# Performance work log

Measured on AMD Instinct MI355X. Metric: run time of the kernel, lower is better.

Reference implementation:

```python
import jax, jax.numpy as jnp
import numpy as np

D_MODEL = 1024
B, S = 4, 4096


def setup_inputs() -> dict:
    key = jax.random.key(0)
    k1, k2, k3, k4, k5 = jax.random.split(key, 5)
    lim = 1.0 / np.sqrt(D_MODEL)  # nn.Linear default init range
    x = jax.random.normal(k1, (B, S, D_MODEL), dtype=jnp.float32)
    mask = jnp.ones((B, S), dtype=jnp.float32)
    W_up = jax.random.uniform(k2, (D_MODEL, D_MODEL), jnp.float32, -lim, lim)
    b_up = jax.random.uniform(k3, (D_MODEL,), jnp.float32, -lim, lim)
    W_f = jax.random.uniform(k4, (D_MODEL, D_MODEL), jnp.float32, -lim, lim)
    b_f = jax.random.uniform(k5, (D_MODEL,), jnp.float32, -lim, lim)
    decay_param = jnp.zeros((1,), dtype=jnp.float32)
    return {"x": x, "mask": mask, "W_up": W_up, "b_up": b_up,
            "W_f": W_f, "b_f": b_f, "decay_param": decay_param}


def _decay_scan(u, decay):
    # h_t = decay * h_{t-1} + u_t  along axis=1, via associative scan.
    # Element: (a, b) representing h -> a*h + b; compose: (a1*a2, b1*a2 + b2).
    a = jnp.broadcast_to(decay, u.shape)

    def combine(c1, c2):
        a1, b1 = c1
        a2, b2 = c2
        return a1 * a2, b1 * a2 + b2

    _, h = jax.lax.associative_scan(combine, (a, u), axis=1)
    return h


def reference(x, mask, W_up, b_up, W_f, b_f, decay_param):
    decay = jax.nn.sigmoid(decay_param)[0]
    # u_i = mask_i * linear_update(x_i)
    u = (jnp.einsum('bsd,ed->bse', x, W_up) + b_up) * mask[..., None]
    # h_t = sum_{i<=t} decay^(t-i) * u_i  (exponential-decay recurrence)
    h = _decay_scan(u, decay)
    return jnp.einsum('bsd,ed->bse', h, W_f) + b_f
```

## Files before the change

kernel.cpp:

```cpp
#include <hip/hip_runtime.h>
#include <hip/hip_bf16.h>
#include <cstdint>
#include <cstddef>

#define DMODEL 1024
#define BATCH  4
#define SEQ    4096
#define BSROWS (BATCH*SEQ)
#define CHUNK  16
#define NCHUNK (SEQ/CHUNK)
#define NCH_T  (BATCH*NCHUNK)

typedef __attribute__((ext_vector_type(8))) short bf16x8;
typedef __attribute__((ext_vector_type(4))) float f32x4;


__device__ __forceinline__ unsigned short f2bf(float f) {
  union { float f; uint32_t u; } v; v.f = f;
  uint32_t u = v.u;
  u += 0x7FFFu + ((u >> 16) & 1u);
  return (unsigned short)(u >> 16);
}

__device__ __forceinline__ float sigmoid_dev(const float* dp) {
  return 1.0f / (1.0f + expf(-dp[0]));
}

typedef __attribute__((address_space(1))) void void_g;
typedef __attribute__((address_space(3))) void void_l;

__device__ __forceinline__ void gl2lds16(const void* g, void* l) {
  __builtin_amdgcn_global_load_lds((void_g*)g, (void_l*)l, 16, 0, 0);
}

__device__ __forceinline__ void kloop64(
    const unsigned short* __restrict__ A, const unsigned short* __restrict__ B,
    int m0, int n0, f32x4 acc[2][2],
    unsigned short* As, unsigned short* Bs, int tid) {
  int lane = tid & 63, w = tid >> 6, wm = w & 1, wn = w >> 1;
  int quad = lane >> 4, l16 = lane & 15;
  int r = tid >> 3, cch = tid & 7;
  int g = cch ^ (r & 7);

  auto stage = [&](int t, int slot) {
    int k0 = t * 64;
    unsigned short* dA = As + slot * 4096;
    unsigned short* dB = Bs + slot * 4096;
    gl2lds16(A + (size_t)(m0 + r) * DMODEL + k0 + g * 8,      dA + r * 64 + cch * 8);
    gl2lds16(A + (size_t)(m0 + 32 + r) * DMODEL + k0 + g * 8, dA + (32 + r) * 64 + cch * 8);
    gl2lds16(B + (size_t)(n0 + r) * DMODEL + k0 + g * 8,      dB + r * 64 + cch * 8);
    gl2lds16(B + (size_t)(n0 + 32 + r) * DMODEL + k0 + g * 8, dB + (32 + r) * 64 + cch * 8);
  };
  auto compute = [&](int slot) {
    const bf16x8* Av = (const bf16x8*)(As + slot * 4096);
    const bf16x8* Bv = (const bf16x8*)(Bs + slot * 4096);
    #pragma unroll
    for (int kk = 0; kk < 2; ++kk) {
      bf16x8 af[2], bfr[2];
      #pragma unroll
      for (int i = 0; i < 2; ++i) {
        int rowA = wm * 32 + i * 16 + l16;
        af[i]  = Av[rowA * 8 + ((kk * 4 + quad) ^ (l16 & 7))];
        int rowB = wn * 32 + i * 16 + l16;
        bfr[i] = Bv[rowB * 8 + ((kk * 4 + quad) ^ (l16 & 7))];
      }
      __builtin_amdgcn_s_setprio(1);
      #pragma unroll
      for (int i = 0; i < 2; ++i)
        #pragma unroll
        for (int j = 0; j < 2; ++j)
          acc[i][j] = __builtin_amdgcn_mfma_f32_16x16x32_bf16(af[i], bfr[j], acc[i][j], 0, 0, 0);
      __builtin_amdgcn_s_setprio(0);
    }
  };

  stage(0, 0); stage(1, 1);
  asm volatile("s_waitcnt vmcnt(4)" ::: "memory");
  __builtin_amdgcn_s_barrier();
  asm volatile("" ::: "memory");
  int cur = 0;
  for (int t = 0; t < 14; ++t) {
    int ns = cur + 2; if (ns >= 3) ns -= 3;
    stage(t + 2, ns);
    compute(cur);
    asm volatile("s_waitcnt vmcnt(4)" ::: "memory");
    __builtin_amdgcn_s_barrier();
    asm volatile("" ::: "memory");
    cur = (cur == 2) ? 0 : cur + 1;
  }
  compute(cur);
  asm volatile("s_waitcnt vmcnt(0)" ::: "memory");
  __builtin_amdgcn_s_barrier();
  asm volatile("" ::: "memory");
  cur = (cur == 2) ? 0 : cur + 1;
  compute(cur);
}

__global__ __launch_bounds__(256) void prep_scan(
    const float* __restrict__ x, const float* __restrict__ mask,
    const float* __restrict__ dp,
    unsigned short* __restrict__ hv, float* __restrict__ carry,
    float* __restrict__ lbeta, float* __restrict__ cbeta) {
  int blk = blockIdx.x;
  int tid = threadIdx.x;
  float decay = sigmoid_dev(dp);
  int b = blk >> 8, c = blk & 255;
  int base = b * SEQ + c * CHUNK;
  const float4* xp = (const float4*)(x + (size_t)base * DMODEL);
  const float4* mp4 = (const float4*)(mask + base);
  float mreg[16];
  #pragma unroll
  for (int q = 0; q < 4; ++q) {
    float4 t = mp4[q];
    mreg[q * 4 + 0] = t.x; mreg[q * 4 + 1] = t.y;
    mreg[q * 4 + 2] = t.z; mreg[q * 4 + 3] = t.w;
  }

  {
    float hb = 0.f;
    #pragma unroll
    for (int i = 0; i < 16; ++i) {
      float nv = decay * hb + mreg[i];
      hb = (tid >= i) ? nv : hb;
    }
    if (tid < 16) {
      lbeta[base + tid] = hb;
      if (tid == 15) cbeta[blk] = hb;
    }
  }

  float4 x0 = xp[tid];
  float4 x1 = xp[256 + tid];
  float4 h = make_float4(0.f, 0.f, 0.f, 0.f);
  #pragma unroll
  for (int s = 0; s < CHUNK; ++s) {
    float4 cur = x0;
    x0 = x1;
    if (s + 2 < CHUNK) x1 = xp[(size_t)(s + 2) * 256 + tid];
    float m = mreg[s];
    h.x = decay * h.x + m * cur.x;
    h.y = decay * h.y + m * cur.y;
    h.z = decay * h.z + m * cur.z;
    h.w = decay * h.w + m * cur.w;
    ushort4 o;
    o.x = f2bf(h.x); o.y = f2bf(h.y); o.z = f2bf(h.z); o.w = f2bf(h.w);
    ((ushort4*)hv)[(size_t)(base + s) * 256 + tid] = o;
  }
  ((float4*)carry)[(size_t)blk * 256 + tid] = h;
}

__global__ __launch_bounds__(256) void prep_misc(
    const float* __restrict__ W_up, const float* __restrict__ b_up,
    const float* __restrict__ W_f,
    unsigned short* __restrict__ Wf_bf, unsigned short* __restrict__ WupT,
    float* __restrict__ bb) {
  __shared__ float tile[32][33];
  int blk = blockIdx.x;
  int tid = threadIdx.x;
  if (blk < 256) {
    int w = tid >> 6, lane = tid & 63;
    int e = blk * 4 + w;
    const float4* row4 = (const float4*)(W_f + (size_t)e * DMODEL);
    const float4* bup4 = (const float4*)b_up;
    ushort4* out4 = (ushort4*)(Wf_bf + (size_t)e * DMODEL);
    float s = 0.f;
    #pragma unroll
    for (int q = 0; q < 4; ++q) {
      float4 v  = row4[q * 64 + lane];
      float4 bu = bup4[q * 64 + lane];
      ushort4 o;
      o.x = f2bf(v.x); o.y = f2bf(v.y); o.z = f2bf(v.z); o.w = f2bf(v.w);
      out4[q * 64 + lane] = o;
      s += v.x * bu.x + v.y * bu.y + v.z * bu.z + v.w * bu.w;
    }
    #pragma unroll
    for (int off = 32; off; off >>= 1) s += __shfl_down(s, off);
    if (lane == 0) bb[e] = s;
  } else {
    int id = blk - 256;
    int bx = id & 31, by = id >> 5;
    int tx = tid & 31, ty = tid >> 5;
    int xx = bx * 32 + tx;
    int y0 = by * 32;
    for (int j = ty; j < 32; j += 8)
      tile[j][tx] = W_up[(size_t)(y0 + j) * DMODEL + xx];
    __syncthreads();
    int dd = tid >> 3;
    int c4 = (tid & 7) * 4;
    ushort4 o;
    o.x = f2bf(tile[c4 + 0][dd]);
    o.y = f2bf(tile[c4 + 1][dd]);
    o.z = f2bf(tile[c4 + 2][dd]);
    o.w = f2bf(tile[c4 + 3][dd]);
    *(ushort4*)(WupT + (size_t)(bx * 32 + dd) * DMODEL + y0 + c4) = o;
  }
}

__global__ __launch_bounds__(256) void mid2_kernel(
    const unsigned short* __restrict__ Wf_bf,
    const unsigned short* __restrict__ WupT,
    unsigned short* __restrict__ Wc,
    const float* __restrict__ carry, const float* __restrict__ cbeta,
    const float* __restrict__ dp,
    unsigned short* __restrict__ Pbf, float* __restrict__ pbeta) {
  __shared__ unsigned short As[3 * 64 * 64];
  __shared__ unsigned short Bs[3 * 64 * 64];
  int tid = threadIdx.x;
  if (blockIdx.x < 256) {
    int mt = blockIdx.x >> 4, nt = blockIdx.x & 15;
    f32x4 acc[2][2] = {};
    kloop64(Wf_bf, WupT, mt * 64, nt * 64, acc, As, Bs, tid);
    int lane = tid & 63, w = tid >> 6, wm = w & 1, wn = w >> 1;
    int quad = lane >> 4, l16 = lane & 15;
    #pragma unroll
    for (int j = 0; j < 2; ++j) {
      int col = nt * 64 + wn * 32 + j * 16 + l16;
      #pragma unroll
      for (int i = 0; i < 2; ++i) {
        int rowb = mt * 64 + wm * 32 + i * 16 + quad * 4;
        #pragma unroll
        for (int rr = 0; rr < 4; ++rr)
          Wc[(size_t)(rowb + rr) * DMODEL + col] = f2bf(acc[i][j][rr]);
      }
    }
  } else {
    float decay = sigmoid_dev(dp);
    float dL = powf(decay, (float)CHUNK);
    int gid = (blockIdx.x - 256) * 256 + tid;
    int b = gid >> 10, dd = gid & 1023;
    float P = 0.f;
    for (int c0 = 0; c0 < NCHUNK; c0 += 8) {
      float v[8];
      #pragma unroll
      for (int j = 0; j < 8; ++j)
        v[j] = carry[(size_t)(b * NCHUNK + c0 + j) * DMODEL + dd];
      #pragma unroll
      for (int j = 0; j < 8; ++j) {
        Pbf[(size_t)(b * NCHUNK + c0 + j) * DMODEL + dd] = f2bf(P);
        P = dL * P + v[j];
      }
    }
    if (dd == 0) {
      float Pb = 0.f;
      for (int c0 = 0; c0 < NCHUNK; c0 += 16) {
        float v[16];
        #pragma unroll
        for (int j = 0; j < 16; ++j) v[j] = cbeta[b * NCHUNK + c0 + j];
        #pragma unroll
        for (int j = 0; j < 16; ++j) {
          pbeta[b * NCHUNK + c0 + j] = Pb;
          Pb = dL * Pb + v[j];
        }
      }
    }
  }
}

__global__ __launch_bounds__(512) void gemm_main(
    const unsigned short* __restrict__ A,
    const unsigned short* __restrict__ Bm,
    const unsigned short* __restrict__ Pbf,
    const float* __restrict__ pbeta,
    const float* __restrict__ lbeta,
    const float* __restrict__ bb,
    const float* __restrict__ bias_f,
    const float* __restrict__ dp,
    float* __restrict__ out) {
  __shared__ unsigned short As[2 * 256 * 64];
  __shared__ unsigned short Bs[2 * 256 * 64];
  __shared__ unsigned short Ps[2 * 16 * 64];
  __shared__ float dpow[CHUNK];
  const int TSLOT = 256 * 64;
  const int PSLOT = 16 * 64;
  int tid = threadIdx.x;
  if (tid < CHUNK) {
    float decay = sigmoid_dev(dp);
    dpow[tid] = powf(decay, (float)(tid + 1));
  }

  int lane = tid & 63, wid = tid >> 6;
  int wm = wid >> 2, wn = wid & 3;
  int quad = lane >> 4, l16 = lane & 15;
  int r = tid >> 3, cch = tid & 7;
  int g = cch ^ (r & 7);

  int bid = blockIdx.x;
  int xcd = bid & 7, jb = bid >> 3;
  int m0 = (xcd * 8 + (jb >> 2)) * 256;
  int n0 = (jb & 3) * 256;
  int chunk0 = m0 >> 4;

  f32x4 acc[8][4] = {};
  f32x4 Pacc[4] = {};

  auto stageT = [&](int t, int p) {
    int k0 = t * 64;
    unsigned short* dA = As + p * TSLOT;
    unsigned short* dB = Bs + p * TSLOT;
    #pragma unroll
    for (int q = 0; q < 4; ++q)
      gl2lds16(A + (size_t)(m0 + q * 64 + r) * DMODEL + k0 + g * 8,
               dA + (q * 64 + r) * 64 + cch * 8);
    #pragma unroll
    for (int q = 0; q < 4; ++q)
      gl2lds16(Bm + (size_t)(n0 + q * 64 + r) * DMODEL + k0 + g * 8,
               dB + (q * 64 + r) * 64 + cch * 8);
    if (wid < 2) {
      int rp = wid * 8 + (lane >> 3), cp = lane & 7;
      int gp = cp ^ (rp & 7);
      gl2lds16(Pbf + (size_t)(chunk0 + rp) * DMODEL + k0 + gp * 8,
               Ps + p * PSLOT + (wid * 64 + lane) * 8);
    }
  };
  auto compute = [&](int p) {
    const bf16x8* Av = (const bf16x8*)(As + p * TSLOT);
    const bf16x8* Bv = (const bf16x8*)(Bs + p * TSLOT);
    const bf16x8* Pv = (const bf16x8*)(Ps + p * PSLOT);
    #pragma unroll
    for (int kk = 0; kk < 2; ++kk) {
      bf16x8 bfr[4];
      #pragma unroll
      for (int j = 0; j < 4; ++j) {
        int rowB = wn * 64 + j * 16 + l16;
        bfr[j] = Bv[rowB * 8 + ((kk * 4 + quad) ^ (l16 & 7))];
      }
      bf16x8 pf = Pv[l16 * 8 + ((kk * 4 + quad) ^ (l16 & 7))];
      __builtin_amdgcn_s_setprio(1);
      #pragma unroll
      for (int j = 0; j < 4; ++j)
        Pacc[j] = __builtin_amdgcn_mfma_f32_16x16x32_bf16(pf, bfr[j], Pacc[j], 0, 0, 0);
      __builtin_amdgcn_s_setprio(0);
      #pragma unroll
      for (int i = 0; i < 8; ++i) {
        int rowA = wm * 128 + i * 16 + l16;
        bf16x8 af = Av[rowA * 8 + ((kk * 4 + quad) ^ (l16 & 7))];
        __builtin_amdgcn_s_setprio(1);
        #pragma unroll
        for (int j = 0; j < 4; ++j)
          acc[i][j] = __builtin_amdgcn_mfma_f32_16x16x32_bf16(af, bfr[j], acc[i][j], 0, 0, 0);
        __builtin_amdgcn_s_setprio(0);
      }
    }
  };

  stageT(0, 0);
  __syncthreads();

  for (int t = 0; t < 15; ++t) {
    int p = t & 1;
    stageT(t + 1, p ^ 1);
    compute(p);
    asm volatile("s_waitcnt vmcnt(0)" ::: "memory");
    __builtin_amdgcn_s_barrier();
    asm volatile("" ::: "memory");
  }
  compute(1);

  float* Plds = (float*)As;
  if (wm == 0) {
    #pragma unroll
    for (int j = 0; j < 4; ++j)
      #pragma unroll
      for (int rr = 0; rr < 4; ++rr)
        Plds[(quad * 4 + rr) * 256 + wn * 64 + j * 16 + l16] = Pacc[j][rr];
  }
  __syncthreads();

  float bbv[4], bfv[4];
  #pragma unroll
  for (int j = 0; j < 4; ++j) {
    int col = n0 + wn * 64 + j * 16 + l16;
    bbv[j] = bb[col];
    bfv[j] = bias_f[col];
  }
  #pragma unroll
  for (int i = 0; i < 8; ++i) {
    int chl = wm * 8 + i;
    float pb = pbeta[chunk0 + chl];
    #pragma unroll
    for (int rr = 0; rr < 4; ++rr) {
      int row = m0 + wm * 128 + i * 16 + quad * 4 + rr;
      float lb  = lbeta[row];
      float dpw = dpow[row & (CHUNK - 1)];
      float* outRow = out + (size_t)row * DMODEL;
      #pragma unroll
      for (int j = 0; j < 4; ++j) {
        int col = n0 + wn * 64 + j * 16 + l16;
        float po = Plds[chl * 256 + wn * 64 + j * 16 + l16] + pb * bbv[j];
        outRow[col] = acc[i][j][rr] + dpw * po + lb * bbv[j] + bfv[j];
      }
    }
  }
}


extern "C" void kernel_launch(void* const* d_in, const int* in_sizes, int n_in,
                              void* d_out, int out_size, void* d_ws, size_t ws_size,
                              hipStream_t stream) {
  const float* x    = (const float*)d_in[0];
  const float* mask = (const float*)d_in[1];
  const float* W_up = (const float*)d_in[2];
  const float* b_up = (const float*)d_in[3];
  const float* W_f  = (const float*)d_in[4];
  const float* b_f  = (const float*)d_in[5];
  const float* dp   = (const float*)d_in[6];
  float* out = (float*)d_out;

  char* ws = (char*)d_ws;
  unsigned short* hv    = (unsigned short*)(ws);
  unsigned short* Wc    = (unsigned short*)(ws + 33554432);
  unsigned short* Wf_bf = (unsigned short*)(ws + 35651584);
  unsigned short* WupT  = (unsigned short*)(ws + 37748736);
  float* carry  = (float*)(ws + 39845888);
  unsigned short* Pbf = (unsigned short*)(ws + 44040192);
  float* lbeta  = (float*)(ws + 46137344);
  float* cbeta  = (float*)(ws + 46202880);
  float* pbeta  = (float*)(ws + 46206976);
  float* bb     = (float*)(ws + 46211072);

  prep_scan<<<1024, 256, 0, stream>>>(x, mask, dp, hv, carry, lbeta, cbeta);
  prep_misc<<<1280, 256, 0, stream>>>(W_up, b_up, W_f, Wf_bf, WupT, bb);
  mid2_kernel<<<272, 256, 0, stream>>>(Wf_bf, WupT, Wc, carry, cbeta, dp,
                                       Pbf, pbeta);
  gemm_main<<<256, 512, 0, stream>>>(hv, Wc, Pbf, pbeta, lbeta, bb, b_f, dp, out);
}
```

Measured before the change: 195.9 us.

## Fuse all four stages into one cooperative persistent kernel with grid syncs

Merges the four separate launches (scan prep, weight prep, weight-combine GEMM plus carry scan, main GEMM) into a single cooperative kernel of 256 blocks of 512 threads, with grid.sync between phases. The goal is to remove launch gaps and tail effects between the small kernels. It also replaces the serial per-batch pbeta scan with a warp-level parallel scan and deepens the x prefetch in the chunk scan from 2 to 4 rows. The cost is fewer concurrent blocks in the prep phases (256 instead of 1024 or 1280), two grid-wide barriers, and the constraint that all blocks must be co-resident.

```diff
diff --git a/kernel.cpp b/kernel.cpp
--- a/kernel.cpp
+++ b/kernel.cpp
@@ -1,7 +1,10 @@
 #include <hip/hip_runtime.h>
+#include <hip/hip_cooperative_groups.h>
 #include <hip/hip_bf16.h>
 #include <cstdint>
 #include <cstddef>
+
+namespace cg = cooperative_groups;
 
 #define DMODEL 1024
 #define BATCH  4
@@ -96,15 +99,12 @@
   compute(cur);
 }
 
-__global__ __launch_bounds__(256) void prep_scan(
+__device__ __forceinline__ void scan_chunk(
+    int ch, int ltid, float decay,
     const float* __restrict__ x, const float* __restrict__ mask,
-    const float* __restrict__ dp,
     unsigned short* __restrict__ hv, float* __restrict__ carry,
     float* __restrict__ lbeta, float* __restrict__ cbeta) {
-  int blk = blockIdx.x;
-  int tid = threadIdx.x;
-  float decay = sigmoid_dev(dp);
-  int b = blk >> 8, c = blk & 255;
+  int b = ch >> 8, c = ch & 255;
   int base = b * SEQ + c * CHUNK;
   const float4* xp = (const float4*)(x + (size_t)base * DMODEL);
   const float4* mp4 = (const float4*)(mask + base);
@@ -115,28 +115,24 @@
     mreg[q * 4 + 0] = t.x; mreg[q * 4 + 1] = t.y;
     mreg[q * 4 + 2] = t.z; mreg[q * 4 + 3] = t.w;
   }
-
   {
     float hb = 0.f;
     #pragma unroll
     for (int i = 0; i < 16; ++i) {
       float nv = decay * hb + mreg[i];
-      hb = (tid >= i) ? nv : hb;
-    }
-    if (tid < 16) {
-      lbeta[base + tid] = hb;
-      if (tid == 15) cbeta[blk] = hb;
-    }
-  }
-
-  float4 x0 = xp[tid];
-  float4 x1 = xp[256 + tid];
+      hb = (ltid >= i) ? nv : hb;
+    }
+    if (ltid < 16) {
+      lbeta[base + ltid] = hb;
+      if (ltid == 15) cbeta[ch] = hb;
+    }
+  }
+  float4 x0 = xp[ltid], x1 = xp[256 + ltid], x2 = xp[512 + ltid], x3 = xp[768 + ltid];
   float4 h = make_float4(0.f, 0.f, 0.f, 0.f);
   #pragma unroll
   for (int s = 0; s < CHUNK; ++s) {
-    float4 cur = x0;
-    x0 = x1;
-    if (s + 2 < CHUNK) x1 = xp[(size_t)(s + 2) * 256 + tid];
+    float4 cur = x0; x0 = x1; x1 = x2; x2 = x3;
+    if (s + 4 < CHUNK) x3 = xp[(size_t)(s + 4) * 256 + ltid];
     float m = mreg[s];
     h.x = decay * h.x + m * cur.x;
     h.y = decay * h.y + m * cur.y;
@@ -144,127 +140,21 @@
     h.w = decay * h.w + m * cur.w;
     ushort4 o;
     o.x = f2bf(h.x); o.y = f2bf(h.y); o.z = f2bf(h.z); o.w = f2bf(h.w);
-    ((ushort4*)hv)[(size_t)(base + s) * 256 + tid] = o;
-  }
-  ((float4*)carry)[(size_t)blk * 256 + tid] = h;
-}
-
-__global__ __launch_bounds__(256) void prep_misc(
+    ((ushort4*)hv)[(size_t)(base + s) * 256 + ltid] = o;
+  }
+  ((float4*)carry)[(size_t)ch * 256 + ltid] = h;
+}
+
+__global__ __launch_bounds__(512) void mega(
+    const float* __restrict__ x, const float* __restrict__ mask,
     const float* __restrict__ W_up, const float* __restrict__ b_up,
-    const float* __restrict__ W_f,
+    const float* __restrict__ W_f, const float* __restrict__ bias_f,
+    const float* __restrict__ dp,
+    unsigned short* __restrict__ hv, float* __restrict__ carry,
     unsigned short* __restrict__ Wf_bf, unsigned short* __restrict__ WupT,
-    float* __restrict__ bb) {
-  __shared__ float tile[32][33];
-  int blk = blockIdx.x;
-  int tid = threadIdx.x;
-  if (blk < 256) {
-    int w = tid >> 6, lane = tid & 63;
-    int e = blk * 4 + w;
-    const float4* row4 = (const float4*)(W_f + (size_t)e * DMODEL);
-    const float4* bup4 = (const float4*)b_up;
-    ushort4* out4 = (ushort4*)(Wf_bf + (size_t)e * DMODEL);
-    float s = 0.f;
-    #pragma unroll
-    for (int q = 0; q < 4; ++q) {
-      float4 v  = row4[q * 64 + lane];
-      float4 bu = bup4[q * 64 + lane];
-      ushort4 o;
-      o.x = f2bf(v.x); o.y = f2bf(v.y); o.z = f2bf(v.z); o.w = f2bf(v.w);
-      out4[q * 64 + lane] = o;
-      s += v.x * bu.x + v.y * bu.y + v.z * bu.z + v.w * bu.w;
-    }
-    #pragma unroll
-    for (int off = 32; off; off >>= 1) s += __shfl_down(s, off);
-    if (lane == 0) bb[e] = s;
-  } else {
-    int id = blk - 256;
-    int bx = id & 31, by = id >> 5;
-    int tx = tid & 31, ty = tid >> 5;
-    int xx = bx * 32 + tx;
-    int y0 = by * 32;
-    for (int j = ty; j < 32; j += 8)
-      tile[j][tx] = W_up[(size_t)(y0 + j) * DMODEL + xx];
-    __syncthreads();
-    int dd = tid >> 3;
-    int c4 = (tid & 7) * 4;
-    ushort4 o;
-    o.x = f2bf(tile[c4 + 0][dd]);
-    o.y = f2bf(tile[c4 + 1][dd]);
-    o.z = f2bf(tile[c4 + 2][dd]);
-    o.w = f2bf(tile[c4 + 3][dd]);
-    *(ushort4*)(WupT + (size_t)(bx * 32 + dd) * DMODEL + y0 + c4) = o;
-  }
-}
-
-__global__ __launch_bounds__(256) void mid2_kernel(
-    const unsigned short* __restrict__ Wf_bf,
-    const unsigned short* __restrict__ WupT,
-    unsigned short* __restrict__ Wc,
-    const float* __restrict__ carry, const float* __restrict__ cbeta,
-    const float* __restrict__ dp,
-    unsigned short* __restrict__ Pbf, float* __restrict__ pbeta) {
-  __shared__ unsigned short As[3 * 64 * 64];
-  __shared__ unsigned short Bs[3 * 64 * 64];
-  int tid = threadIdx.x;
-  if (blockIdx.x < 256) {
-    int mt = blockIdx.x >> 4, nt = blockIdx.x & 15;
-    f32x4 acc[2][2] = {};
-    kloop64(Wf_bf, WupT, mt * 64, nt * 64, acc, As, Bs, tid);
-    int lane = tid & 63, w = tid >> 6, wm = w & 1, wn = w >> 1;
-    int quad = lane >> 4, l16 = lane & 15;
-    #pragma unroll
-    for (int j = 0; j < 2; ++j) {
-      int col = nt * 64 + wn * 32 + j * 16 + l16;
-      #pragma unroll
-      for (int i = 0; i < 2; ++i) {
-        int rowb = mt * 64 + wm * 32 + i * 16 + quad * 4;
-        #pragma unroll
-        for (int rr = 0; rr < 4; ++rr)
-          Wc[(size_t)(rowb + rr) * DMODEL + col] = f2bf(acc[i][j][rr]);
-      }
-    }
-  } else {
-    float decay = sigmoid_dev(dp);
-    float dL = powf(decay, (float)CHUNK);
-    int gid = (blockIdx.x - 256) * 256 + tid;
-    int b = gid >> 10, dd = gid & 1023;
-    float P = 0.f;
-    for (int c0 = 0; c0 < NCHUNK; c0 += 8) {
-      float v[8];
-      #pragma unroll
-      for (int j = 0; j < 8; ++j)
-        v[j] = carry[(size_t)(b * NCHUNK + c0 + j) * DMODEL + dd];
-      #pragma unroll
-      for (int j = 0; j < 8; ++j) {
-        Pbf[(size_t)(b * NCHUNK + c0 + j) * DMODEL + dd] = f2bf(P);
-        P = dL * P + v[j];
-      }
-    }
-    if (dd == 0) {
-      float Pb = 0.f;
-      for (int c0 = 0; c0 < NCHUNK; c0 += 16) {
-        float v[16];
-        #pragma unroll
-        for (int j = 0; j < 16; ++j) v[j] = cbeta[b * NCHUNK + c0 + j];
-        #pragma unroll
-        for (int j = 0; j < 16; ++j) {
-          pbeta[b * NCHUNK + c0 + j] = Pb;
-          Pb = dL * Pb + v[j];
-        }
-      }
-    }
-  }
-}
-
-__global__ __launch_bounds__(512) void gemm_main(
-    const unsigned short* __restrict__ A,
-    const unsigned short* __restrict__ Bm,
-    const unsigned short* __restrict__ Pbf,
-    const float* __restrict__ pbeta,
-    const float* __restrict__ lbeta,
-    const float* __restrict__ bb,
-    const float* __restrict__ bias_f,
-    const float* __restrict__ dp,
+    unsigned short* __restrict__ Wc, unsigned short* __restrict__ Pbf,
+    float* __restrict__ lbeta, float* __restrict__ cbeta,
+    float* __restrict__ pbeta, float* __restrict__ bb,
     float* __restrict__ out) {
   __shared__ unsigned short As[2 * 256 * 64];
   __shared__ unsigned short Bs[2 * 256 * 64];
@@ -273,121 +163,261 @@
   const int TSLOT = 256 * 64;
   const int PSLOT = 16 * 64;
   int tid = threadIdx.x;
-  if (tid < CHUNK) {
-    float decay = sigmoid_dev(dp);
-    dpow[tid] = powf(decay, (float)(tid + 1));
-  }
-
-  int lane = tid & 63, wid = tid >> 6;
-  int wm = wid >> 2, wn = wid & 3;
-  int quad = lane >> 4, l16 = lane & 15;
-  int r = tid >> 3, cch = tid & 7;
-  int g = cch ^ (r & 7);
-
-  int bid = blockIdx.x;
-  int xcd = bid & 7, jb = bid >> 3;
-  int m0 = (xcd * 8 + (jb >> 2)) * 256;
-  int n0 = (jb & 3) * 256;
-  int chunk0 = m0 >> 4;
-
-  f32x4 acc[8][4] = {};
-  f32x4 Pacc[4] = {};
-
-  auto stageT = [&](int t, int p) {
-    int k0 = t * 64;
-    unsigned short* dA = As + p * TSLOT;
-    unsigned short* dB = Bs + p * TSLOT;
+  int blk = blockIdx.x;
+  float decay = sigmoid_dev(dp);
+  cg::grid_group grid = cg::this_grid();
+
+  {
+    int g = tid >> 8;
+    int ltid = tid & 255;
+    scan_chunk(blk * 4 + g * 2 + 0, ltid, decay, x, mask, hv, carry, lbeta, cbeta);
+    scan_chunk(blk * 4 + g * 2 + 1, ltid, decay, x, mask, hv, carry, lbeta, cbeta);
+
+    if (tid < 256) {
+      int w = tid >> 6, lane = tid & 63;
+      int e = blk * 4 + w;
+      const float4* row4 = (const float4*)(W_f + (size_t)e * DMODEL);
+      const float4* bup4 = (const float4*)b_up;
+      ushort4* out4 = (ushort4*)(Wf_bf + (size_t)e * DMODEL);
+      float s = 0.f;
+      #pragma unroll
+      for (int q = 0; q < 4; ++q) {
+        float4 v  = row4[q * 64 + lane];
+        float4 bu = bup4[q * 64 + lane];
+        ushort4 o;
+        o.x = f2bf(v.x); o.y = f2bf(v.y); o.z = f2bf(v.z); o.w = f2bf(v.w);
+        out4[q * 64 + lane] = o;
+        s += v.x * bu.x + v.y * bu.y + v.z * bu.z + v.w * bu.w;
+      }
+      #pragma unroll
+      for (int off = 32; off; off >>= 1) s += __shfl_down(s, off);
+      if (lane == 0) bb[e] = s;
+    } else {
+      int wv = (tid >> 6) - 4, lane = tid & 63;
+      int id = blk * 4 + wv;
+      int bx = id & 31, by = id >> 5;
+      int x0c = bx * 32, y0 = by * 32;
+      float* tw = (float*)As + wv * (32 * 33);
+      #pragma unroll
+      for (int p = 0; p < 4; ++p) {
+        int idx = p * 64 + lane;
+        int rr = idx >> 3, q = idx & 7;
+        float4 t = *(const float4*)(W_up + (size_t)(y0 + rr) * DMODEL + x0c + q * 4);
+        tw[rr * 33 + q * 4 + 0] = t.x;
+        tw[rr * 33 + q * 4 + 1] = t.y;
+        tw[rr * 33 + q * 4 + 2] = t.z;
+        tw[rr * 33 + q * 4 + 3] = t.w;
+      }
+      asm volatile("s_waitcnt lgkmcnt(0)" ::: "memory");
+      __builtin_amdgcn_sched_barrier(0);
+      #pragma unroll
+      for (int p = 0; p < 4; ++p) {
+        int idx = p * 64 + lane;
+        int d = idx >> 3, q = idx & 7;
+        ushort4 o;
+        o.x = f2bf(tw[(q * 4 + 0) * 33 + d]);
+        o.y = f2bf(tw[(q * 4 + 1) * 33 + d]);
+        o.z = f2bf(tw[(q * 4 + 2) * 33 + d]);
+        o.w = f2bf(tw[(q * 4 + 3) * 33 + d]);
+        *(ushort4*)(WupT + (size_t)(x0c + d) * DMODEL + y0 + q * 4) = o;
+      }
+    }
+  }
+  __syncthreads();
+  __threadfence();
+  grid.sync();
+  __threadfence();
+
+  {
+    unsigned short* As2 = As;
+    unsigned short* Bs2 = As + 3 * 4096;
+    if (tid < 256) {
+      int mt = blk >> 4, nt = blk & 15;
+      f32x4 acc[2][2] = {};
+      kloop64(Wf_bf, WupT, mt * 64, nt * 64, acc, As2, Bs2, tid);
+      int lane = tid & 63, w = tid >> 6, wm = w & 1, wn = w >> 1;
+      int quad = lane >> 4, l16 = lane & 15;
+      #pragma unroll
+      for (int j = 0; j < 2; ++j) {
+        int col = nt * 64 + wn * 32 + j * 16 + l16;
+        #pragma unroll
+        for (int i = 0; i < 2; ++i) {
+          int rowb = mt * 64 + wm * 32 + i * 16 + quad * 4;
+          #pragma unroll
+          for (int rr = 0; rr < 4; ++rr)
+            Wc[(size_t)(rowb + rr) * DMODEL + col] = f2bf(acc[i][j][rr]);
+        }
+      }
+    } else {
+      float dL = powf(decay, (float)CHUNK);
+      if (blk < 16) {
+        int gid = blk * 256 + (tid - 256);
+        int b = gid >> 10, dd = gid & 1023;
+        float P = 0.f;
+        for (int c0 = 0; c0 < NCHUNK; c0 += 8) {
+          float v[8];
+          #pragma unroll
+          for (int j = 0; j < 8; ++j)
+            v[j] = carry[(size_t)(b * NCHUNK + c0 + j) * DMODEL + dd];
+          #pragma unroll
+          for (int j = 0; j < 8; ++j) {
+            Pbf[(size_t)(b * NCHUNK + c0 + j) * DMODEL + dd] = f2bf(P);
+            P = dL * P + v[j];
+          }
+          if (c0 & 8) __builtin_amdgcn_s_barrier();
+        }
+      } else if (blk == 16) {
+        int wv = (tid >> 6) - 4, lane = tid & 63;
+        float F = dL * dL; F = F * F;
+        float c0v = cbeta[wv * NCHUNK + lane * 4 + 0];
+        float c1v = cbeta[wv * NCHUNK + lane * 4 + 1];
+        float c2v = cbeta[wv * NCHUNK + lane * 4 + 2];
+        float c3v = cbeta[wv * NCHUNK + lane * 4 + 3];
+        float p1 = c0v;
+        float p2 = dL * p1 + c1v;
+        float p3 = dL * p2 + c2v;
+        float T  = dL * p3 + c3v;
+        float s = T, f = F;
+        #pragma unroll
+        for (int off = 1; off < 64; off <<= 1) {
+          float u = __shfl_up(s, off);
+          if (lane >= off) s += f * u;
+          f = f * f;
+        }
+        float E = __shfl_up(s, 1);
+        if (lane == 0) E = 0.f;
+        float q0 = E;
+        float q1 = dL * q0 + c0v;
+        float q2 = dL * q1 + c1v;
+        float q3 = dL * q2 + c2v;
+        pbeta[wv * NCHUNK + lane * 4 + 0] = q0;
+        pbeta[wv * NCHUNK + lane * 4 + 1] = q1;
+        pbeta[wv * NCHUNK + lane * 4 + 2] = q2;
+        pbeta[wv * NCHUNK + lane * 4 + 3] = q3;
+        for (int i = 0; i < 16; ++i) __builtin_amdgcn_s_barrier();
+      } else {
+        for (int i = 0; i < 16; ++i) __builtin_amdgcn_s_barrier();
+      }
+    }
+  }
+  __syncthreads();
+  __threadfence();
+  grid.sync();
+  __threadfence();
+
+  {
+    if (tid < CHUNK) dpow[tid] = powf(decay, (float)(tid + 1));
+
+    int lane = tid & 63, wid = tid >> 6;
+    int wm = wid >> 2, wn = wid & 3;
+    int quad = lane >> 4, l16 = lane & 15;
+    int r = tid >> 3, cch = tid & 7;
+    int g = cch ^ (r & 7);
+
+    int xcd = blk & 7, jb = blk >> 3;
+    int m0 = (xcd * 8 + (jb >> 2)) * 256;
+    int n0 = (jb & 3) * 256;
+    int chunk0 = m0 >> 4;
+
+    f32x4 acc[8][4] = {};
+    f32x4 Pacc[4] = {};
+
+    auto stageT = [&](int t, int p) {
+      int k0 = t * 64;
+      unsigned short* dA = As + p * TSLOT;
+      unsigned short* dB = Bs + p * TSLOT;
+      #pragma unroll
+      for (int q = 0; q < 4; ++q)
+        gl2lds16(hv + (size_t)(m0 + q * 64 + r) * DMODEL + k0 + g * 8,
+                 dA + (q * 64 + r) * 64 + cch * 8);
+      #pragma unroll
+      for (int q = 0; q < 4; ++q)
+        gl2lds16(Wc + (size_t)(n0 + q * 64 + r) * DMODEL + k0 + g * 8,
+                 dB + (q * 64 + r) * 64 + cch * 8);
+      if (wid < 2) {
+        int rp = wid * 8 + (lane >> 3), cp = lane & 7;
+        int gp = cp ^ (rp & 7);
+        gl2lds16(Pbf + (size_t)(chunk0 + rp) * DMODEL + k0 + gp * 8,
+                 Ps + p * PSLOT + (wid * 64 + lane) * 8);
+      }
+    };
+    auto compute = [&](int p) {
+      const bf16x8* Av = (const bf16x8*)(As + p * TSLOT);
+      const bf16x8* Bv = (const bf16x8*)(Bs + p * TSLOT);
+      const bf16x8* Pv = (const bf16x8*)(Ps + p * PSLOT);
+      #pragma unroll
+      for (int kk = 0; kk < 2; ++kk) {
+        bf16x8 bfr[4];
+        #pragma unroll
+        for (int j = 0; j < 4; ++j) {
+          int rowB = wn * 64 + j * 16 + l16;
+          bfr[j] = Bv[rowB * 8 + ((kk * 4 + quad) ^ (l16 & 7))];
+        }
+        bf16x8 pf = Pv[l16 * 8 + ((kk * 4 + quad) ^ (l16 & 7))];
+        __builtin_amdgcn_s_setprio(1);
+        #pragma unroll
+        for (int j = 0; j < 4; ++j)
+          Pacc[j] = __builtin_amdgcn_mfma_f32_16x16x32_bf16(pf, bfr[j], Pacc[j], 0, 0, 0);
+        __builtin_amdgcn_s_setprio(0);
+        #pragma unroll
+        for (int i = 0; i < 8; ++i) {
+          int rowA = wm * 128 + i * 16 + l16;
+          bf16x8 af = Av[rowA * 8 + ((kk * 4 + quad) ^ (l16 & 7))];
+          __builtin_amdgcn_s_setprio(1);
+          #pragma unroll
+          for (int j = 0; j < 4; ++j)
+            acc[i][j] = __builtin_amdgcn_mfma_f32_16x16x32_bf16(af, bfr[j], acc[i][j], 0, 0, 0);
+          __builtin_amdgcn_s_setprio(0);
+        }
+      }
+    };
+
+    stageT(0, 0);
+    __syncthreads();
+
+    for (int t = 0; t < 15; ++t) {
+      int p = t & 1;
+      stageT(t + 1, p ^ 1);
+      compute(p);
+      asm volatile("s_waitcnt vmcnt(0)" ::: "memory");
+      __builtin_amdgcn_s_barrier();
+      asm volatile("" ::: "memory");
+    }
+    compute(1);
+
+    float* Plds = (float*)As;
+    if (wm == 0) {
+      #pragma unroll
+      for (int j = 0; j < 4; ++j)
+        #pragma unroll
+        for (int rr = 0; rr < 4; ++rr)
+          Plds[(quad * 4 + rr) * 256 + wn * 64 + j * 16 + l16] = Pacc[j][rr];
+    }
+    __syncthreads();
+
+    float bbv[4], bfv[4];
     #pragma unroll
-    for (int q = 0; q < 4; ++q)
-      gl2lds16(A + (size_t)(m0 + q * 64 + r) * DMODEL + k0 + g * 8,
-               dA + (q * 64 + r) * 64 + cch * 8);
+    for (int j = 0; j < 4; ++j) {
+      int col = n0 + wn * 64 + j * 16 + l16;
+      bbv[j] = bb[col];
+      bfv[j] = bias_f[col];
+    }
     #pragma unroll
-    for (int q = 0; q < 4; ++q)
-      gl2lds16(Bm + (size_t)(n0 + q * 64 + r) * DMODEL + k0 + g * 8,
-               dB + (q * 64 + r) * 64 + cch * 8);
-    if (wid < 2) {
-      int rp = wid * 8 + (lane >> 3), cp = lane & 7;
-      int gp = cp ^ (rp & 7);
-      gl2lds16(Pbf + (size_t)(chunk0 + rp) * DMODEL + k0 + gp * 8,
-               Ps + p * PSLOT + (wid * 64 + lane) * 8);
-    }
-  };
-  auto compute = [&](int p) {
-    const bf16x8* Av = (const bf16x8*)(As + p * TSLOT);
-    const bf16x8* Bv = (const bf16x8*)(Bs + p * TSLOT);
-    const bf16x8* Pv = (const bf16x8*)(Ps + p * PSLOT);
-    #pragma unroll
-    for (int kk = 0; kk < 2; ++kk) {
-      bf16x8 bfr[4];
-      #pragma unroll
-      for (int j = 0; j < 4; ++j) {
-        int rowB = wn * 64 + j * 16 + l16;
-        bfr[j] = Bv[rowB * 8 + ((kk * 4 + quad) ^ (l16 & 7))];
-      }
-      bf16x8 pf = Pv[l16 * 8 + ((kk * 4 + quad) ^ (l16 & 7))];
-      __builtin_amdgcn_s_setprio(1);
-      #pragma unroll
-      for (int j = 0; j < 4; ++j)
-        Pacc[j] = __builtin_amdgcn_mfma_f32_16x16x32_bf16(pf, bfr[j], Pacc[j], 0, 0, 0);
-      __builtin_amdgcn_s_setprio(0);
-      #pragma unroll
-      for (int i = 0; i < 8; ++i) {
-        int rowA = wm * 128 + i * 16 + l16;
-        bf16x8 af = Av[rowA * 8 + ((kk * 4 + quad) ^ (l16 & 7))];
-        __builtin_amdgcn_s_setprio(1);
-        #pragma unroll
-        for (int j = 0; j < 4; ++j)
-          acc[i][j] = __builtin_amdgcn_mfma_f32_16x16x32_bf16(af, bfr[j], acc[i][j], 0, 0, 0);
-        __builtin_amdgcn_s_setprio(0);
-      }
-    }
-  };
-
-  stageT(0, 0);
-  __syncthreads();
-
-  for (int t = 0; t < 15; ++t) {
-    int p = t & 1;
-    stageT(t + 1, p ^ 1);
-    compute(p);
-    asm volatile("s_waitcnt vmcnt(0)" ::: "memory");
-    __builtin_amdgcn_s_barrier();
-    asm volatile("" ::: "memory");
-  }
-  compute(1);
-
-  float* Plds = (float*)As;
-  if (wm == 0) {
-    #pragma unroll
-    for (int j = 0; j < 4; ++j)
-      #pragma unroll
-      for (int rr = 0; rr < 4; ++rr)
-        Plds[(quad * 4 + rr) * 256 + wn * 64 + j * 16 + l16] = Pacc[j][rr];
-  }
-  __syncthreads();
-
-  float bbv[4], bfv[4];
-  #pragma unroll
-  for (int j = 0; j < 4; ++j) {
-    int col = n0 + wn * 64 + j * 16 + l16;
-    bbv[j] = bb[col];
-    bfv[j] = bias_f[col];
-  }
-  #pragma unroll
-  for (int i = 0; i < 8; ++i) {
-    int chl = wm * 8 + i;
-    float pb = pbeta[chunk0 + chl];
-    #pragma unroll
-    for (int rr = 0; rr < 4; ++rr) {
-      int row = m0 + wm * 128 + i * 16 + quad * 4 + rr;
-      float lb  = lbeta[row];
-      float dpw = dpow[row & (CHUNK - 1)];
-      float* outRow = out + (size_t)row * DMODEL;
-      #pragma unroll
-      for (int j = 0; j < 4; ++j) {
-        int col = n0 + wn * 64 + j * 16 + l16;
-        float po = Plds[chl * 256 + wn * 64 + j * 16 + l16] + pb * bbv[j];
-        outRow[col] = acc[i][j][rr] + dpw * po + lb * bbv[j] + bfv[j];
+    for (int i = 0; i < 8; ++i) {
+      int chl = wm * 8 + i;
+      float pb = pbeta[chunk0 + chl];
+      #pragma unroll
+      for (int rr = 0; rr < 4; ++rr) {
+        int row = m0 + wm * 128 + i * 16 + quad * 4 + rr;
+        float lb  = lbeta[row];
+        float dpw = dpow[row & (CHUNK - 1)];
+        float* outRow = out + (size_t)row * DMODEL;
+        #pragma unroll
+        for (int j = 0; j < 4; ++j) {
+          int col = n0 + wn * 64 + j * 16 + l16;
+          float po = Plds[chl * 256 + wn * 64 + j * 16 + l16] + pb * bbv[j];
+          outRow[col] = acc[i][j][rr] + dpw * po + lb * bbv[j] + bfv[j];
+        }
       }
     }
   }
@@ -418,9 +448,13 @@
   float* pbeta  = (float*)(ws + 46206976);
   float* bb     = (float*)(ws + 46211072);
 
-  prep_scan<<<1024, 256, 0, stream>>>(x, mask, dp, hv, carry, lbeta, cbeta);
-  prep_misc<<<1280, 256, 0, stream>>>(W_up, b_up, W_f, Wf_bf, WupT, bb);
-  mid2_kernel<<<272, 256, 0, stream>>>(Wf_bf, WupT, Wc, carry, cbeta, dp,
-                                       Pbf, pbeta);
-  gemm_main<<<256, 512, 0, stream>>>(hv, Wc, Pbf, pbeta, lbeta, bb, b_f, dp, out);
-}
+  void* kargs[] = {
+    (void*)&x, (void*)&mask, (void*)&W_up, (void*)&b_up, (void*)&W_f,
+    (void*)&b_f, (void*)&dp,
+    (void*)&hv, (void*)&carry, (void*)&Wf_bf, (void*)&WupT, (void*)&Wc,
+    (void*)&Pbf, (void*)&lbeta, (void*)&cbeta, (void*)&pbeta, (void*)&bb,
+    (void*)&out
+  };
+  hipLaunchCooperativeKernel((const void*)mega, dim3(256), dim3(512),
+                             kargs, 0, stream);
+}
```

Measured after the change: 453.1 us. 131% more time.
